# Kernel tuning notes

Measured on AMD Instinct MI355X. Metric: run time of the kernel, lower is better.

The kernel has to match this reference:

```python
import jax, jax.numpy as jnp
import numpy as np

EPS = 1e-12  # F.normalize eps

def _l2norm(v, axis):
    n = jnp.sqrt(jnp.sum(v * v, axis=axis, keepdims=True))
    return v / jnp.maximum(n, EPS)

def setup_inputs() -> dict:
    key = jax.random.key(0)
    ks = jax.random.split(key, 4)
    B, N, C, centers = 128, 196, 768, 64
    x = jax.random.normal(ks[0], (B, N, C), dtype=jnp.float32)
    k_c = jax.random.normal(ks[1], (C, centers), dtype=jnp.float32)
    v_c = jax.random.normal(ks[2], (centers, N, N), dtype=jnp.float32)
    proj_w = jax.random.normal(ks[3], (C, C), dtype=jnp.float32) * (C ** -0.5)
    proj_b = jnp.zeros((C,), dtype=jnp.float32)
    return {"x": x, "k_c": k_c, "v_c": v_c, "proj_w": proj_w, "proj_b": proj_b}

def reference(x, k_c, v_c, proj_w, proj_b):
    # x: (B, N, C); k_c: (C, centers); v_c: (centers, N, N)
    C = x.shape[-1]
    scale = C ** -0.5
    q = x.mean(axis=1)                                  # (B, C)
    attn = _l2norm(q, -1) @ _l2norm(k_c, 0)             # (B, centers)
    attn = jax.nn.softmax(attn * scale, axis=-1)        # (B, centers)
    # attention-weighted mixture of basis matrices: (B,centers)x(centers,N*N) GEMM
    v = jnp.einsum('bc,cnm->bnm', attn, v_c)            # (B, N, N)
    out = jnp.einsum('bnm,bmd->bnd', v, x)              # (B, N, C)
    out = out @ proj_w.T + proj_b                        # Linear(dim, dim)
    return out
```

## Files before the change

### kernel.cpp

```cpp
#include <hip/hip_runtime.h>
#include <hip/hip_bf16.h>


#define NB   128
#define NN   196
#define NC   768
#define NCEN 64
#define RPAD 256
#define KPAD 224
#define BGRP 32

using bf16x8 = __attribute__((ext_vector_type(8))) short;
using f32x4  = __attribute__((ext_vector_type(4))) float;

__device__ __forceinline__ void async_copy16(const void* g, void* l) {
    __builtin_amdgcn_global_load_lds((const __attribute__((address_space(1))) void*)g,
                                     (__attribute__((address_space(3))) void*)l, 16, 0, 0);
}

__global__ __launch_bounds__(256)
void convert_x_kernel(const float* __restrict__ x, __hip_bfloat16* __restrict__ x_bf,
                      float* __restrict__ q_part) {
    int b = blockIdx.x, chunk = blockIdx.y, part = blockIdx.z, t = threadIdx.x;
    int c = chunk * 256 + t;
    const float* xp = x + (size_t)b * NN * NC + c;
    __hip_bfloat16* xo = x_bf + (size_t)b * RPAD * NC + c;
    float s = 0.f;
    int m0 = part * 49;
#pragma unroll 7
    for (int m = m0; m < m0 + 49; ++m) {
        float v = xp[(size_t)m * NC];
        s += v;
        xo[(size_t)m * NC] = __float2bfloat16(v);
    }
    q_part[((size_t)part * NB + b) * NC + c] = s;
}

__global__ __launch_bounds__(256)
void convert_w_kernel(const float* __restrict__ w, __hip_bfloat16* __restrict__ w_bf) {
    int i = blockIdx.x * 256 + threadIdx.x;
    if (i < NC * NC) w_bf[i] = __float2bfloat16(w[i]);
}

__global__ __launch_bounds__(256)
void attn_kernel(const float* __restrict__ q_part, const float* __restrict__ k_c,
                 float* __restrict__ attn) {
    const float SCALE = 0.03608439182435161f;
    int b = blockIdx.x, t = threadIdx.x;
    __shared__ float qs[NC];
    __shared__ float red[256];
    __shared__ float pd[4][NCEN];
    __shared__ float pk[4][NCEN];

    const size_t PS = (size_t)NB * NC;
    for (int i = t; i < NC; i += 256) {
        size_t idx = (size_t)b * NC + i;
        qs[i] = (q_part[idx] + q_part[PS + idx] + q_part[2 * PS + idx] + q_part[3 * PS + idx])
                * (1.0f / (float)NN);
    }
    __syncthreads();

    float s = 0.f;
    for (int i = t; i < NC; i += 256) { float v = qs[i]; s += v * v; }
    red[t] = s;
    __syncthreads();
    for (int o = 128; o > 0; o >>= 1) {
        if (t < o) red[t] += red[t + o];
        __syncthreads();
    }
    float qn = sqrtf(red[0]);

    int j = t & 63, part = t >> 6;
    float d = 0.f, kk = 0.f;
    int c0 = part * 192;
    for (int c = c0; c < c0 + 192; ++c) {
        float kv = k_c[c * NCEN + j];
        d += kv * qs[c];
        kk += kv * kv;
    }
    pd[part][j] = d;
    pk[part][j] = kk;
    __syncthreads();

    if (t < NCEN) {
        float dot = pd[0][t] + pd[1][t] + pd[2][t] + pd[3][t];
        float kn  = sqrtf(pk[0][t] + pk[1][t] + pk[2][t] + pk[3][t]);
        float lg = dot / (fmaxf(qn, 1e-12f) * fmaxf(kn, 1e-12f)) * SCALE;
        float mx = lg;
        for (int o = 32; o > 0; o >>= 1) mx = fmaxf(mx, __shfl_xor(mx, o, 64));
        float e = expf(lg - mx);
        float sum = e;
        for (int o = 32; o > 0; o >>= 1) sum += __shfl_xor(sum, o, 64);
        attn[b * NCEN + t] = e / sum;
    }
}

__global__ __launch_bounds__(256)
void mix_kernel(const float* __restrict__ attn, const float* __restrict__ v_c,
                __hip_bfloat16* __restrict__ v_pad) {
    int n = blockIdx.x;
    int g = blockIdx.y;
    int m = threadIdx.x;
    if (m >= KPAD) return;
    size_t base = (size_t)n * KPAD + m;
    if (m >= NN) {
        __hip_bfloat16 z = __float2bfloat16(0.f);
#pragma unroll
        for (int bb = 0; bb < BGRP; ++bb)
            v_pad[(size_t)(g * BGRP + bb) * RPAD * KPAD + base] = z;
        return;
    }
    float vc[NCEN];
    const float* vp = v_c + (size_t)n * NN + m;
#pragma unroll
    for (int c = 0; c < NCEN; ++c) vc[c] = vp[(size_t)c * NN * NN];
    const float* ab = attn + (size_t)g * BGRP * NCEN;
    for (int bb = 0; bb < BGRP; ++bb) {
        float acc = 0.f;
#pragma unroll
        for (int c = 0; c < NCEN; ++c) acc += ab[bb * NCEN + c] * vc[c];
        v_pad[(size_t)(g * BGRP + bb) * RPAD * KPAD + base] = __float2bfloat16(acc);
    }
}

template <int BK, bool OUT_BF16, int MODE>
__global__ __launch_bounds__(256)
void gemm_nt(const __hip_bfloat16* __restrict__ A, size_t strideA,
             const __hip_bfloat16* __restrict__ Bm, size_t strideB,
             void* __restrict__ Cout, size_t strideC,
             const float* __restrict__ bias,
             int lda, int ldb, int ldc, int K, int Mstore, int Nstore) {
    int id = blockIdx.x;
    int bm, bn, bb;
    if (MODE == 0) {
        int xcd = id & 7, idx = id >> 3;
        bm = idx % 6;
        int grp = xcd * 32 + idx / 6;
        bn = grp & 1; bb = grp >> 1;
    } else {
        int xcd = id & 7, idx = id >> 3;
        bb = xcd * 16 + idx / 12;
        int r = idx % 12;
        bm = r & 1; bn = r >> 1;
    }
    const unsigned short* Ab = (const unsigned short*)A + (size_t)bb * strideA + (size_t)bm * 128 * lda;
    const unsigned short* Bb = (const unsigned short*)Bm + (size_t)bb * strideB + (size_t)bn * 128 * ldb;

    __shared__ __align__(16) unsigned short sA[128 * BK];
    __shared__ __align__(16) unsigned short sB[128 * BK];

    int tid = threadIdx.x;
    int wave = tid >> 6, lane = tid & 63;
    int wr = wave >> 1, wc = wave & 1;
    int lrow = lane & 15, quad = lane >> 4;

    constexpr int CH  = BK / 8;
    constexpr int RPI = 64 / CH;
    constexpr int NI  = 32 / RPI;
    int srow = lane / CH;
    int sc   = lane % CH;
    int lc   = (BK == 64) ? (sc ^ (srow & 7)) : sc;

    const unsigned short* ga[NI];
    const unsigned short* gb[NI];
    unsigned short* la[NI];
    unsigned short* lb[NI];
#pragma unroll
    for (int i = 0; i < NI; ++i) {
        int row = wave * 32 + i * RPI + srow;
        ga[i] = Ab + (size_t)row * lda + lc * 8;
        gb[i] = Bb + (size_t)row * ldb + lc * 8;
        la[i] = &sA[(wave * 32 + i * RPI) * BK];
        lb[i] = &sB[(wave * 32 + i * RPI) * BK];
    }

    f32x4 acc[4][4] = {};

    for (int k0 = 0; k0 < K; k0 += BK) {
        __syncthreads();
#pragma unroll
        for (int i = 0; i < NI; ++i) async_copy16(ga[i] + k0, la[i]);
#pragma unroll
        for (int i = 0; i < NI; ++i) async_copy16(gb[i] + k0, lb[i]);
        __syncthreads();

#pragma unroll
        for (int kh = 0; kh < BK / 32; ++kh) {
            int pcbase = (BK == 64) ? ((kh * 4 + quad) ^ (lrow & 7)) : quad;
            bf16x8 af[4], bfr[4];
#pragma unroll
            for (int i = 0; i < 4; ++i)
                af[i] = *(const bf16x8*)(&sA[(wr * 64 + i * 16 + lrow) * BK + pcbase * 8]);
#pragma unroll
            for (int j = 0; j < 4; ++j)
                bfr[j] = *(const bf16x8*)(&sB[(wc * 64 + j * 16 + lrow) * BK + pcbase * 8]);
#pragma unroll
            for (int i = 0; i < 4; ++i)
#pragma unroll
                for (int j = 0; j < 4; ++j)
                    acc[i][j] = __builtin_amdgcn_mfma_f32_16x16x32_bf16(af[i], bfr[j], acc[i][j], 0, 0, 0);
        }
    }

    size_t cbase = (size_t)bb * strideC;
#pragma unroll
    for (int i = 0; i < 4; ++i) {
        int row0 = bm * 128 + wr * 64 + i * 16 + quad * 4;
#pragma unroll
        for (int j = 0; j < 4; ++j) {
            int col = bn * 128 + wc * 64 + j * 16 + lrow;
            if (col < Nstore) {
                float badd = bias ? bias[col] : 0.f;
#pragma unroll
                for (int r = 0; r < 4; ++r) {
                    int row = row0 + r;
                    if (row < Mstore) {
                        float v = acc[i][j][r] + badd;
                        if (OUT_BF16)
                            ((__hip_bfloat16*)Cout)[cbase + (size_t)row * ldc + col] = __float2bfloat16(v);
                        else
                            ((float*)Cout)[cbase + (size_t)row * ldc + col] = v;
                    }
                }
            }
        }
    }
}

extern "C" void kernel_launch(void* const* d_in, const int* in_sizes, int n_in,
                              void* d_out, int out_size, void* d_ws, size_t ws_size,
                              hipStream_t stream) {
    const float* x      = (const float*)d_in[0];
    const float* k_c    = (const float*)d_in[1];
    const float* v_c    = (const float*)d_in[2];
    const float* proj_w = (const float*)d_in[3];
    const float* proj_b = (const float*)d_in[4];
    float* out = (float*)d_out;

    char* ws = (char*)d_ws;
    size_t off = 0;
    auto alloc = [&](size_t bytes) {
        void* p = ws + off;
        off = (off + bytes + 255) & ~(size_t)255;
        return p;
    };
    __hip_bfloat16* x_bf  = (__hip_bfloat16*)alloc((size_t)NB * RPAD * NC * 2);
    __hip_bfloat16* w_bf  = (__hip_bfloat16*)alloc((size_t)NC * NC * 2);
    __hip_bfloat16* xp_t  = (__hip_bfloat16*)alloc((size_t)NB * NC * KPAD * 2);
    __hip_bfloat16* v_pad = (__hip_bfloat16*)alloc((size_t)NB * RPAD * KPAD * 2);
    float* q_part = (float*)alloc((size_t)4 * NB * NC * 4);
    float* attn   = (float*)alloc((size_t)NB * NCEN * 4);

    convert_x_kernel<<<dim3(NB, 3, 4), 256, 0, stream>>>(x, x_bf, q_part);
    convert_w_kernel<<<dim3((NC * NC + 255) / 256), 256, 0, stream>>>(proj_w, w_bf);
    attn_kernel<<<dim3(NB), 256, 0, stream>>>(q_part, k_c, attn);
    mix_kernel<<<dim3(NN, NB / BGRP), 256, 0, stream>>>(attn, v_c, v_pad);

    gemm_nt<64, true, 0><<<dim3(1536), 256, 0, stream>>>(
        w_bf, 0, x_bf, (size_t)RPAD * NC, xp_t, (size_t)NC * KPAD, nullptr,
        NC, NC, KPAD, NC, NC, KPAD);

    gemm_nt<32, false, 1><<<dim3(1536), 256, 0, stream>>>(
        v_pad, (size_t)RPAD * KPAD, xp_t, (size_t)NC * KPAD, out, (size_t)NN * NC, proj_b,
        KPAD, KPAD, NC, KPAD, NN, NC);
}
```

Measured before the change: 324.6 us.

## Use 128x256 GEMM tiles with BK=64 and pad K dimension to 256

Both batched GEMMs switch from 128x128 to 128x256 output tiles with a fixed BK=64 and swizzled LDS layout, halving the grid to 768 blocks and doubling per-wave accumulators. KPAD grows from 224 to 256 so the second GEMM can also use BK=64 and a full 256-wide N tile in the first GEMM. This aims for more data reuse per LDS load, paid for with extra zero-padded K work, more registers (lower occupancy), and fewer blocks to fill the GPU.

```diff
diff --git a/kernel.cpp b/kernel.cpp
--- a/kernel.cpp
+++ b/kernel.cpp
@@ -7,7 +7,7 @@
 #define NC   768
 #define NCEN 64
 #define RPAD 256
-#define KPAD 224
+#define KPAD 256
 #define BGRP 32
 
 using bf16x8 = __attribute__((ext_vector_type(8))) short;
@@ -101,7 +101,6 @@
     int n = blockIdx.x;
     int g = blockIdx.y;
     int m = threadIdx.x;
-    if (m >= KPAD) return;
     size_t base = (size_t)n * KPAD + m;
     if (m >= NN) {
         __hip_bfloat16 z = __float2bfloat16(0.f);
@@ -123,7 +122,7 @@
     }
 }
 
-template <int BK, bool OUT_BF16, int MODE>
+template <bool OUT_BF16, int MODE>
 __global__ __launch_bounds__(256)
 void gemm_nt(const __hip_bfloat16* __restrict__ A, size_t strideA,
              const __hip_bfloat16* __restrict__ Bm, size_t strideB,
@@ -131,73 +130,69 @@
              const float* __restrict__ bias,
              int lda, int ldb, int ldc, int K, int Mstore, int Nstore) {
     int id = blockIdx.x;
-    int bm, bn, bb;
-    if (MODE == 0) {
-        int xcd = id & 7, idx = id >> 3;
-        bm = idx % 6;
-        int grp = xcd * 32 + idx / 6;
-        bn = grp & 1; bb = grp >> 1;
-    } else {
-        int xcd = id & 7, idx = id >> 3;
-        bb = xcd * 16 + idx / 12;
-        int r = idx % 12;
-        bm = r & 1; bn = r >> 1;
-    }
+    int xcd = id & 7, idx = id >> 3;
+    int bb = xcd * 16 + idx / 6;
+    int r = idx % 6;
+    int bm, bn;
+    if (MODE == 0) { bm = r; bn = 0; }
+    else           { bm = r & 1; bn = r >> 1; }
+
     const unsigned short* Ab = (const unsigned short*)A + (size_t)bb * strideA + (size_t)bm * 128 * lda;
-    const unsigned short* Bb = (const unsigned short*)Bm + (size_t)bb * strideB + (size_t)bn * 128 * ldb;
-
-    __shared__ __align__(16) unsigned short sA[128 * BK];
-    __shared__ __align__(16) unsigned short sB[128 * BK];
+    const unsigned short* Bb = (const unsigned short*)Bm + (size_t)bb * strideB + (size_t)bn * 256 * ldb;
+
+    __shared__ __align__(16) unsigned short sA[128 * 64];
+    __shared__ __align__(16) unsigned short sB[256 * 64];
 
     int tid = threadIdx.x;
     int wave = tid >> 6, lane = tid & 63;
     int wr = wave >> 1, wc = wave & 1;
     int lrow = lane & 15, quad = lane >> 4;
 
-    constexpr int CH  = BK / 8;
-    constexpr int RPI = 64 / CH;
-    constexpr int NI  = 32 / RPI;
-    int srow = lane / CH;
-    int sc   = lane % CH;
-    int lc   = (BK == 64) ? (sc ^ (srow & 7)) : sc;
-
-    const unsigned short* ga[NI];
-    const unsigned short* gb[NI];
-    unsigned short* la[NI];
-    unsigned short* lb[NI];
-#pragma unroll
-    for (int i = 0; i < NI; ++i) {
-        int row = wave * 32 + i * RPI + srow;
+    int srow = lane >> 3;
+    int sc   = lane & 7;
+    int lc   = sc ^ srow;
+
+    const unsigned short* ga[4];
+    unsigned short* la[4];
+#pragma unroll
+    for (int i = 0; i < 4; ++i) {
+        int row = wave * 32 + i * 8 + srow;
         ga[i] = Ab + (size_t)row * lda + lc * 8;
+        la[i] = &sA[(wave * 32 + i * 8) * 64];
+    }
+    const unsigned short* gb[8];
+    unsigned short* lb[8];
+#pragma unroll
+    for (int i = 0; i < 8; ++i) {
+        int row = wave * 64 + i * 8 + srow;
         gb[i] = Bb + (size_t)row * ldb + lc * 8;
-        la[i] = &sA[(wave * 32 + i * RPI) * BK];
-        lb[i] = &sB[(wave * 32 + i * RPI) * BK];
-    }
-
-    f32x4 acc[4][4] = {};
-
-    for (int k0 = 0; k0 < K; k0 += BK) {
+        lb[i] = &sB[(wave * 64 + i * 8) * 64];
+    }
+
+    f32x4 acc[4][8] = {};
+
+    for (int k0 = 0; k0 < K; k0 += 64) {
         __syncthreads();
 #pragma unroll
-        for (int i = 0; i < NI; ++i) async_copy16(ga[i] + k0, la[i]);
-#pragma unroll
-        for (int i = 0; i < NI; ++i) async_copy16(gb[i] + k0, lb[i]);
+        for (int i = 0; i < 4; ++i) async_copy16(ga[i] + k0, la[i]);
+#pragma unroll
+        for (int i = 0; i < 8; ++i) async_copy16(gb[i] + k0, lb[i]);
         __syncthreads();
 
 #pragma unroll
-        for (int kh = 0; kh < BK / 32; ++kh) {
-            int pcbase = (BK == 64) ? ((kh * 4 + quad) ^ (lrow & 7)) : quad;
-            bf16x8 af[4], bfr[4];
+        for (int kh = 0; kh < 2; ++kh) {
+            int pc = (kh * 4 + quad) ^ (lrow & 7);
+            bf16x8 af[4], bfr[8];
 #pragma unroll
             for (int i = 0; i < 4; ++i)
-                af[i] = *(const bf16x8*)(&sA[(wr * 64 + i * 16 + lrow) * BK + pcbase * 8]);
-#pragma unroll
-            for (int j = 0; j < 4; ++j)
-                bfr[j] = *(const bf16x8*)(&sB[(wc * 64 + j * 16 + lrow) * BK + pcbase * 8]);
+                af[i] = *(const bf16x8*)(&sA[(wr * 64 + i * 16 + lrow) * 64 + pc * 8]);
+#pragma unroll
+            for (int j = 0; j < 8; ++j)
+                bfr[j] = *(const bf16x8*)(&sB[(wc * 128 + j * 16 + lrow) * 64 + pc * 8]);
 #pragma unroll
             for (int i = 0; i < 4; ++i)
 #pragma unroll
-                for (int j = 0; j < 4; ++j)
+                for (int j = 0; j < 8; ++j)
                     acc[i][j] = __builtin_amdgcn_mfma_f32_16x16x32_bf16(af[i], bfr[j], acc[i][j], 0, 0, 0);
         }
     }
@@ -207,15 +202,15 @@
     for (int i = 0; i < 4; ++i) {
         int row0 = bm * 128 + wr * 64 + i * 16 + quad * 4;
 #pragma unroll
-        for (int j = 0; j < 4; ++j) {
-            int col = bn * 128 + wc * 64 + j * 16 + lrow;
+        for (int j = 0; j < 8; ++j) {
+            int col = bn * 256 + wc * 128 + j * 16 + lrow;
             if (col < Nstore) {
                 float badd = bias ? bias[col] : 0.f;
 #pragma unroll
-                for (int r = 0; r < 4; ++r) {
-                    int row = row0 + r;
+                for (int r2 = 0; r2 < 4; ++r2) {
+                    int row = row0 + r2;
                     if (row < Mstore) {
-                        float v = acc[i][j][r] + badd;
+                        float v = acc[i][j][r2] + badd;
                         if (OUT_BF16)
                             ((__hip_bfloat16*)Cout)[cbase + (size_t)row * ldc + col] = __float2bfloat16(v);
                         else
@@ -256,11 +251,11 @@
     attn_kernel<<<dim3(NB), 256, 0, stream>>>(q_part, k_c, attn);
     mix_kernel<<<dim3(NN, NB / BGRP), 256, 0, stream>>>(attn, v_c, v_pad);
 
-    gemm_nt<64, true, 0><<<dim3(1536), 256, 0, stream>>>(
+    gemm_nt<true, 0><<<dim3(768), 256, 0, stream>>>(
         w_bf, 0, x_bf, (size_t)RPAD * NC, xp_t, (size_t)NC * KPAD, nullptr,
         NC, NC, KPAD, NC, NC, KPAD);
 
-    gemm_nt<32, false, 1><<<dim3(1536), 256, 0, stream>>>(
+    gemm_nt<false, 1><<<dim3(768), 256, 0, stream>>>(
         v_pad, (size_t)RPAD * KPAD, xp_t, (size_t)NC * KPAD, out, (size_t)NN * NC, proj_b,
         KPAD, KPAD, NC, KPAD, NN, NC);
 }
```

New measurement: 411.5 us. 1.27x slower.
